# Kernel optimization log

Measured on AMD Instinct MI355X. Metric: run time of the kernel, lower is better.

The kernel has to match this reference:

```python
import jax, jax.numpy as jnp
import numpy as np

EPS = 1e-8

def setup_inputs() -> dict:
    key = jax.random.key(0)
    k1, k2, k3 = jax.random.split(key, 3)
    B, N, C = 4, 2048, 512
    x = jax.random.normal(k1, (B, N, C), dtype=jnp.float32)
    w_qkv = jax.random.normal(k2, (C, 3 * C), dtype=jnp.float32) * (C ** -0.5)
    w_proj = jax.random.normal(k3, (C, C), dtype=jnp.float32) * (C ** -0.5)
    b_proj = jnp.zeros((C,), dtype=jnp.float32)
    alpha = jnp.ones((1,), dtype=jnp.float32)
    beta = jnp.ones((1,), dtype=jnp.float32)
    return {"x": x, "w_qkv": w_qkv, "alpha": alpha, "beta": beta,
            "w_proj": w_proj, "b_proj": b_proj}

def reference(x, w_qkv, alpha, beta, w_proj, b_proj):
    B, N, C = x.shape
    H = 8  # num_heads
    D = C // H  # head_dim = 64
    scale = D ** -0.5
    qkv = (x @ w_qkv).reshape(B, N, 3, H, D)
    q = jnp.transpose(qkv[:, :, 0], (0, 2, 1, 3))  # (B,H,N,D)
    k = jnp.transpose(qkv[:, :, 1], (0, 2, 1, 3))
    v = jnp.transpose(qkv[:, :, 2], (0, 2, 1, 3))
    attn = jnp.einsum('bhnd,bhmd->bhnm', q, k) * scale  # (B,H,N,N)
    # sparse branch: relu^2 sum-normalize
    sp = jnp.square(jax.nn.relu(attn))
    attn_sparse = sp / (sp.sum(axis=-1, keepdims=True) + EPS)
    # dense branch: softmax
    attn_dense = jax.nn.softmax(attn, axis=-1)
    a = jax.nn.sigmoid(alpha)
    b = jax.nn.sigmoid(beta)
    wsum = a + b + EPS
    attn_final = (a / wsum) * attn_sparse + (b / wsum) * attn_dense
    out = jnp.einsum('bhnm,bhmd->bhnd', attn_final, v)  # (B,H,N,D)
    out = jnp.transpose(out, (0, 2, 1, 3)).reshape(B, N, C)
    return out @ w_proj + b_proj
```

## Files before the change

kernel.cpp:

```cpp
#include <hip/hip_runtime.h>

typedef unsigned short u16;
typedef unsigned int   u32;
typedef __attribute__((ext_vector_type(8))) __bf16 bf16x8;
typedef __attribute__((ext_vector_type(4))) float  f32x4;
typedef __attribute__((ext_vector_type(4))) u32    u32x4;

#define AS1q __attribute__((address_space(1)))
#define AS3q __attribute__((address_space(3)))

static __device__ __forceinline__ u16 f2bf(float f) {
    u32 u = __builtin_bit_cast(u32, f);
    u32 r = u + 0x7FFFu + ((u >> 16) & 1u);
    return (u16)(r >> 16);
}

static __device__ __forceinline__ bf16x8 ld16(const u16* p) {
    return __builtin_bit_cast(bf16x8, *(const float4*)(const void*)p);
}

static __device__ __forceinline__ f32x4 mfma16(bf16x8 a, bf16x8 b, f32x4 c) {
    return __builtin_amdgcn_mfma_f32_16x16x32_bf16(a, b, c, 0, 0, 0);
}

static __device__ __forceinline__ void gld16(const u16* g, u16* l) {
    __builtin_amdgcn_global_load_lds((const AS1q u32*)g, (AS3q u32*)l, 16, 0, 0);
}

static __device__ __forceinline__ float exp2_fast(float v) {
    float e;
    asm("v_exp_f32 %0, %1" : "=v"(e) : "v"(v));
    return e;
}

static __device__ __forceinline__ u32 cvtpk(float lo, float hi_) {
    u32 d;
    asm("v_cvt_pk_bf16_f32 %0, %1, %2" : "=v"(d) : "v"(lo), "v"(hi_));
    return d;
}

__global__ __launch_bounds__(256) void k_cast_x(const float* __restrict__ x, u16* __restrict__ xb) {
    int i = blockIdx.x * 256 + threadIdx.x;
    float4 v = ((const float4*)x)[i];
    ushort4 o;
    o.x = f2bf(v.x); o.y = f2bf(v.y); o.z = f2bf(v.z); o.w = f2bf(v.w);
    ((ushort4*)xb)[i] = o;
}

__global__ __launch_bounds__(256) void k_transpose_cast(const float* __restrict__ in, u16* __restrict__ out,
                                                        int K, int Nn) {
    __shared__ float tile[32][33];
    int tx = threadIdx.x & 31, ty = threadIdx.x >> 5;
    int k0 = blockIdx.y * 32, n0 = blockIdx.x * 32;
#pragma unroll
    for (int i = 0; i < 4; ++i)
        tile[ty + i * 8][tx] = in[(k0 + ty + i * 8) * Nn + n0 + tx];
    __syncthreads();
#pragma unroll
    for (int i = 0; i < 4; ++i)
        out[(n0 + ty + i * 8) * K + k0 + tx] = f2bf(tile[tx][ty + i * 8]);
}

static __device__ __forceinline__ void stage128x64(const u16* __restrict__ gbase, int ld,
                                                   u16* lds, int tid) {
    int wid = tid >> 6;
#pragma unroll
    for (int i = 0; i < 4; ++i) {
        int idx = i * 256 + tid;
        int row = idx >> 3, c8 = idx & 7;
        int csw = c8 ^ (row & 7);
        gld16(gbase + row * ld + csw * 8, lds + (i * 256 + wid * 64) * 8);
    }
}

static __device__ __forceinline__ bf16x8 frag(const u16* lds, int row, int col16) {
    return ld16(lds + row * 64 + ((col16 ^ (row & 7)) << 3));
}

__global__ __launch_bounds__(256) void k_gemm_qkv(const u16* __restrict__ xb, const u16* __restrict__ wT,
                                                  u16* __restrict__ Qh, u16* __restrict__ Kh,
                                                  u16* __restrict__ VTh) {
    __shared__ __align__(16) u16 at[128 * 64];
    __shared__ __align__(16) u16 bt[128 * 64];
    int tid = threadIdx.x, lane = tid & 63, wid = tid >> 6;
    int tm = blockIdx.x / 12, tn = blockIdx.x % 12;
    int rb = tm * 128, cb = tn * 128;
    int wr = (wid >> 1) * 64, wc = (wid & 1) * 64;
    int l15 = lane & 15, lhi = lane >> 4;
    f32x4 acc[4][4] = {};
    for (int kk = 0; kk < 512; kk += 64) {
        stage128x64(xb + rb * 512 + kk, 512, at, tid);
        stage128x64(wT + cb * 512 + kk, 512, bt, tid);
        __syncthreads();
        bf16x8 af[4][2], bfr[4][2];
#pragma unroll
        for (int m = 0; m < 4; ++m) {
            int row = wr + m * 16 + l15;
            af[m][0] = frag(at, row, lhi);
            af[m][1] = frag(at, row, 4 + lhi);
        }
#pragma unroll
        for (int n = 0; n < 4; ++n) {
            int row = wc + n * 16 + l15;
            bfr[n][0] = frag(bt, row, lhi);
            bfr[n][1] = frag(bt, row, 4 + lhi);
        }
#pragma unroll
        for (int m = 0; m < 4; ++m)
#pragma unroll
            for (int n = 0; n < 4; ++n) {
                acc[m][n] = mfma16(af[m][0], bfr[n][0], acc[m][n]);
                acc[m][n] = mfma16(af[m][1], bfr[n][1], acc[m][n]);
            }
        __syncthreads();
    }
#pragma unroll
    for (int m = 0; m < 4; ++m)
#pragma unroll
        for (int n = 0; n < 4; ++n)
#pragma unroll
            for (int r = 0; r < 4; ++r) {
                int R  = rb + wr + m * 16 + lhi * 4 + r;
                int Cg = cb + wc + n * 16 + l15;
                int b = R >> 11, nseq = R & 2047;
                int s = Cg >> 9, rm = Cg & 511, h = rm >> 6, d = rm & 63;
                int bh = (b << 3) + h;
                float v = acc[m][n][r];
                if (s == 0)      Qh[(bh * 2048 + nseq) * 64 + d] = f2bf(v * 0.1803368801111244f);
                else if (s == 1) Kh[(bh * 2048 + nseq) * 64 + d] = f2bf(v);
                else             VTh[(bh * 64 + d) * 2048 + nseq] = f2bf(v);
            }
}

#define ATTN_SUB(BUF, KS)                                                        \
    {                                                                            \
        f32x4 s[2][2];                                                           \
        _Pragma("unroll")                                                        \
        for (int kt = 0; kt < 2; ++kt) {                                         \
            int row = (KS)*32 + kap + 2 * kt;                                    \
            const u16* kbp = &kls[BUF][0] + row * 64;                            \
            bf16x8 kf0 = ld16(kbp + ((lhi ^ (row & 7)) << 3));                   \
            bf16x8 kf1 = ld16(kbp + (((4 + lhi) ^ (row & 7)) << 3));             \
            _Pragma("unroll")                                                    \
            for (int qg = 0; qg < 2; ++qg) {                                     \
                s[qg][kt] = mfma16(kf0, qa[qg][0], z);                           \
                s[qg][kt] = mfma16(kf1, qa[qg][1], s[qg][kt]);                   \
            }                                                                    \
        }                                                                        \
        bf16x8 pfd[2], pfs[2];                                                   \
        _Pragma("unroll")                                                        \
        for (int qg = 0; qg < 2; ++qg) {                                         \
            float ed[2][4], ps[2][4];                                            \
            _Pragma("unroll")                                                    \
            for (int kt = 0; kt < 2; ++kt)                                       \
                _Pragma("unroll")                                                \
                for (int r = 0; r < 4; ++r) {                                    \
                    float v = s[qg][kt][r];                                      \
                    float e = exp2_fast(v);                                      \
                    float t = fmaxf(v, 0.f);                                     \
                    ed[kt][r] = e; ps[kt][r] = t * t;                            \
                }                                                                \
            pfd[qg] = __builtin_bit_cast(bf16x8, (u32x4){                        \
                cvtpk(ed[0][0], ed[0][1]), cvtpk(ed[1][0], ed[1][1]),            \
                cvtpk(ed[0][2], ed[0][3]), cvtpk(ed[1][2], ed[1][3])});          \
            pfs[qg] = __builtin_bit_cast(bf16x8, (u32x4){                        \
                cvtpk(ps[0][0], ps[0][1]), cvtpk(ps[1][0], ps[1][1]),            \
                cvtpk(ps[0][2], ps[0][3]), cvtpk(ps[1][2], ps[1][3])});          \
        }                                                                        \
        _Pragma("unroll")                                                        \
        for (int n = 0; n < 4; ++n) {                                            \
            int row = n * 16 + l15;                                              \
            bf16x8 vf = ld16(&vls[BUF][0] + row * 64 +                           \
                             ((((KS)*4 + lhi) ^ (row & 7)) << 3));               \
            _Pragma("unroll")                                                    \
            for (int qg = 0; qg < 2; ++qg) {                                     \
                accd[qg][n] = mfma16(pfd[qg], vf, accd[qg][n]);                  \
                accs[qg][n] = mfma16(pfs[qg], vf, accs[qg][n]);                  \
            }                                                                    \
        }                                                                        \
        _Pragma("unroll")                                                        \
        for (int qg = 0; qg < 2; ++qg) {                                         \
            dend[qg] = mfma16(pfd[qg], onesf, dend[qg]);                         \
            dens[qg] = mfma16(pfs[qg], onesf, dens[qg]);                         \
        }                                                                        \
    }

__global__ __launch_bounds__(256) void k_attn(const u16* __restrict__ Qh, const u16* __restrict__ Kh,
                                              const u16* __restrict__ VTh, const float* __restrict__ alpha,
                                              const float* __restrict__ beta, u16* __restrict__ AO) {
    __shared__ __align__(16) u16 kls[2][64 * 64];
    __shared__ __align__(16) u16 vls[2][64 * 64];
    int tid = threadIdx.x, lane = tid & 63, wid = tid >> 6;
    int l15 = lane & 15, lhi = lane >> 4;
    int wg = (blockIdx.x & 7) * 64 + (blockIdx.x >> 3);
    int bh = wg >> 4;
    int qb = (wg & 15) << 7;
    const u16* Qp = Qh + bh * (2048 * 64);
    const u16* Kp = Kh + bh * (2048 * 64);
    const u16* Vp = VTh + bh * (2048 * 64);
    int qbase = qb + wid * 32;
    bf16x8 qa[2][2];
#pragma unroll
    for (int qg = 0; qg < 2; ++qg) {
        int row = qbase + qg * 16 + l15;
        qa[qg][0] = ld16(Qp + row * 64 + lhi * 8);
        qa[qg][1] = ld16(Qp + row * 64 + 32 + lhi * 8);
    }
    int kap = 8 * (l15 >> 2) + 4 * ((l15 >> 1) & 1) + (l15 & 1);
    f32x4 accd[2][4] = {}, accs[2][4] = {};
    f32x4 dend[2] = {}, dens[2] = {};
    const f32x4 z = {0.f, 0.f, 0.f, 0.f};
    const bf16x8 onesf = __builtin_bit_cast(bf16x8, (u32x4){0x3F803F80u, 0x3F803F80u,
                                                            0x3F803F80u, 0x3F803F80u});

    int srow = tid >> 3, sc8 = tid & 7;
    const u16* kg0 = Kp + srow * 64 + ((sc8 ^ (srow & 7)) << 3);
    const u16* kg1 = Kp + (srow + 32) * 64 + ((sc8 ^ ((srow + 32) & 7)) << 3);
    const u16* vg0 = Vp + srow * 2048 + ((sc8 ^ (srow & 7)) << 3);
    const u16* vg1 = Vp + (srow + 32) * 2048 + ((sc8 ^ ((srow + 32) & 7)) << 3);

    gld16(kg0, &kls[0][0] + tid * 8);
    gld16(kg1, &kls[0][0] + 2048 + tid * 8);
    gld16(vg0, &vls[0][0] + tid * 8);
    gld16(vg1, &vls[0][0] + 2048 + tid * 8);
    int koff = 64 * 64, voff = 64;

    for (int g = 0; g < 32; ++g) {
        int cur = g & 1;
        if (g + 1 < 32) {
            u16* kd = &kls[cur ^ 1][0];
            u16* vd = &vls[cur ^ 1][0];
            gld16(kg0 + koff, kd + tid * 8);
            gld16(kg1 + koff, kd + 2048 + tid * 8);
            gld16(vg0 + voff, vd + tid * 8);
            gld16(vg1 + voff, vd + 2048 + tid * 8);
            koff += 64 * 64; voff += 64;
            asm volatile("s_waitcnt vmcnt(4)" ::: "memory");
        } else {
            asm volatile("s_waitcnt vmcnt(0)" ::: "memory");
        }
        __builtin_amdgcn_s_barrier();
        ATTN_SUB(cur, 0)
        ATTN_SUB(cur, 1)
        asm volatile("" ::: "memory");
        __builtin_amdgcn_s_barrier();
    }
    float sa = 1.f / (1.f + __expf(-alpha[0]));
    float sb = 1.f / (1.f + __expf(-beta[0]));
    float wsum = sa + sb + 1e-8f;
    float wa = sa / wsum, wb = sb / wsum;
    int b = bh >> 3, h = bh & 7;
#pragma unroll
    for (int qg = 0; qg < 2; ++qg) {
        float id[4], isr[4];
#pragma unroll
        for (int r = 0; r < 4; ++r) {
            id[r]  = wb / dend[qg][r];
            isr[r] = wa / (dens[qg][r] + 1e-8f);
        }
#pragma unroll
        for (int n = 0; n < 4; ++n)
#pragma unroll
            for (int r = 0; r < 4; ++r) {
                int R  = b * 2048 + qbase + qg * 16 + lhi * 4 + r;
                int Cg = h * 64 + n * 16 + l15;
                float o = isr[r] * accs[qg][n][r] + id[r] * accd[qg][n][r];
                AO[R * 512 + Cg] = f2bf(o);
            }
    }
}

__global__ __launch_bounds__(256) void k_gemm_proj(const u16* __restrict__ AO, const u16* __restrict__ wT,
                                                   const float* __restrict__ bproj, float* __restrict__ out) {
    __shared__ __align__(16) u16 at[128 * 64];
    __shared__ __align__(16) u16 bt[128 * 64];
    int tid = threadIdx.x, lane = tid & 63, wid = tid >> 6;
    int tm = blockIdx.x >> 2, tn = blockIdx.x & 3;
    int rb = tm * 128, cb = tn * 128;
    int wr = (wid >> 1) * 64, wc = (wid & 1) * 64;
    int l15 = lane & 15, lhi = lane >> 4;
    f32x4 acc[4][4] = {};
    for (int kk = 0; kk < 512; kk += 64) {
        stage128x64(AO + rb * 512 + kk, 512, at, tid);
        stage128x64(wT + cb * 512 + kk, 512, bt, tid);
        __syncthreads();
        bf16x8 af[4][2], bfr[4][2];
#pragma unroll
        for (int m = 0; m < 4; ++m) {
            int row = wr + m * 16 + l15;
            af[m][0] = frag(at, row, lhi);
            af[m][1] = frag(at, row, 4 + lhi);
        }
#pragma unroll
        for (int n = 0; n < 4; ++n) {
            int row = wc + n * 16 + l15;
            bfr[n][0] = frag(bt, row, lhi);
            bfr[n][1] = frag(bt, row, 4 + lhi);
        }
#pragma unroll
        for (int m = 0; m < 4; ++m)
#pragma unroll
            for (int n = 0; n < 4; ++n) {
                acc[m][n] = mfma16(af[m][0], bfr[n][0], acc[m][n]);
                acc[m][n] = mfma16(af[m][1], bfr[n][1], acc[m][n]);
            }
        __syncthreads();
    }
#pragma unroll
    for (int m = 0; m < 4; ++m)
#pragma unroll
        for (int n = 0; n < 4; ++n)
#pragma unroll
            for (int r = 0; r < 4; ++r) {
                int R  = rb + wr + m * 16 + lhi * 4 + r;
                int Cg = cb + wc + n * 16 + l15;
                out[R * 512 + Cg] = acc[m][n][r] + bproj[Cg];
            }
}

extern "C" void kernel_launch(void* const* d_in, const int* in_sizes, int n_in,
                              void* d_out, int out_size, void* d_ws, size_t ws_size,
                              hipStream_t stream) {
    const float* x      = (const float*)d_in[0];
    const float* w_qkv  = (const float*)d_in[1];
    const float* alpha  = (const float*)d_in[2];
    const float* beta   = (const float*)d_in[3];
    const float* w_proj = (const float*)d_in[4];
    const float* b_proj = (const float*)d_in[5];
    float* out = (float*)d_out;
    char* w = (char*)d_ws;
    u16* xb     = (u16*)(w);
    u16* wqkvT  = (u16*)(w + 8388608);
    u16* wprojT = (u16*)(w + 9961472);
    u16* Qh     = (u16*)(w + 10485760);
    u16* Kh     = (u16*)(w + 18874368);
    u16* VTh    = (u16*)(w + 27262976);
    u16* AO     = xb;

    k_cast_x<<<dim3(4096), dim3(256), 0, stream>>>(x, xb);
    k_transpose_cast<<<dim3(48, 16), dim3(256), 0, stream>>>(w_qkv, wqkvT, 512, 1536);
    k_transpose_cast<<<dim3(16, 16), dim3(256), 0, stream>>>(w_proj, wprojT, 512, 512);
    k_gemm_qkv<<<dim3(768), dim3(256), 0, stream>>>(xb, wqkvT, Qh, Kh, VTh);
    k_attn<<<dim3(512), dim3(256), 0, stream>>>(Qh, Kh, VTh, alpha, beta, AO);
    k_gemm_proj<<<dim3(256), dim3(256), 0, stream>>>(AO, wprojT, b_proj, out);
}
```

Baseline: 145.5 us.

## Load K and V fragments straight from global into registers, dropping LDS staging

The attention kernel no longer stages K/V tiles in double-buffered shared memory behind block barriers. Each wave now loads its MFMA K fragments directly from global memory, with a one-step register prefetch, and loads its V fragments just before use. This removes LDS writes, LDS reads and barriers. In exchange, the four waves each fetch the same K/V data redundantly through the cache, V loads are less coalesced and are not prefetched, and the final prefetch reads past the end of the K tile.

```diff
diff --git a/kernel.cpp b/kernel.cpp
--- a/kernel.cpp
+++ b/kernel.cpp
@@ -132,20 +132,19 @@
             }
 }
 
-#define ATTN_SUB(BUF, KS)                                                        \
+#define ATTN_COMPUTE(KF0, KF1, KF2, KF3, VOFF)                                   \
     {                                                                            \
+        bf16x8 vf0 = ld16(vp0 + (VOFF));                                         \
+        bf16x8 vf1 = ld16(vp1 + (VOFF));                                         \
+        bf16x8 vf2 = ld16(vp2 + (VOFF));                                         \
+        bf16x8 vf3 = ld16(vp3 + (VOFF));                                         \
         f32x4 s[2][2];                                                           \
         _Pragma("unroll")                                                        \
-        for (int kt = 0; kt < 2; ++kt) {                                         \
-            int row = (KS)*32 + kap + 2 * kt;                                    \
-            const u16* kbp = &kls[BUF][0] + row * 64;                            \
-            bf16x8 kf0 = ld16(kbp + ((lhi ^ (row & 7)) << 3));                   \
-            bf16x8 kf1 = ld16(kbp + (((4 + lhi) ^ (row & 7)) << 3));             \
-            _Pragma("unroll")                                                    \
-            for (int qg = 0; qg < 2; ++qg) {                                     \
-                s[qg][kt] = mfma16(kf0, qa[qg][0], z);                           \
-                s[qg][kt] = mfma16(kf1, qa[qg][1], s[qg][kt]);                   \
-            }                                                                    \
+        for (int qg = 0; qg < 2; ++qg) {                                         \
+            s[qg][0] = mfma16(KF0, qa[qg][0], z);                                \
+            s[qg][0] = mfma16(KF1, qa[qg][1], s[qg][0]);                         \
+            s[qg][1] = mfma16(KF2, qa[qg][0], z);                                \
+            s[qg][1] = mfma16(KF3, qa[qg][1], s[qg][1]);                         \
         }                                                                        \
         bf16x8 pfd[2], pfs[2];                                                   \
         _Pragma("unroll")                                                        \
@@ -168,18 +167,15 @@
                 cvtpk(ps[0][2], ps[0][3]), cvtpk(ps[1][2], ps[1][3])});          \
         }                                                                        \
         _Pragma("unroll")                                                        \
-        for (int n = 0; n < 4; ++n) {                                            \
-            int row = n * 16 + l15;                                              \
-            bf16x8 vf = ld16(&vls[BUF][0] + row * 64 +                           \
-                             ((((KS)*4 + lhi) ^ (row & 7)) << 3));               \
-            _Pragma("unroll")                                                    \
-            for (int qg = 0; qg < 2; ++qg) {                                     \
-                accd[qg][n] = mfma16(pfd[qg], vf, accd[qg][n]);                  \
-                accs[qg][n] = mfma16(pfs[qg], vf, accs[qg][n]);                  \
-            }                                                                    \
-        }                                                                        \
-        _Pragma("unroll")                                                        \
         for (int qg = 0; qg < 2; ++qg) {                                         \
+            accd[qg][0] = mfma16(pfd[qg], vf0, accd[qg][0]);                     \
+            accs[qg][0] = mfma16(pfs[qg], vf0, accs[qg][0]);                     \
+            accd[qg][1] = mfma16(pfd[qg], vf1, accd[qg][1]);                     \
+            accs[qg][1] = mfma16(pfs[qg], vf1, accs[qg][1]);                     \
+            accd[qg][2] = mfma16(pfd[qg], vf2, accd[qg][2]);                     \
+            accs[qg][2] = mfma16(pfs[qg], vf2, accs[qg][2]);                     \
+            accd[qg][3] = mfma16(pfd[qg], vf3, accd[qg][3]);                     \
+            accs[qg][3] = mfma16(pfs[qg], vf3, accs[qg][3]);                     \
             dend[qg] = mfma16(pfd[qg], onesf, dend[qg]);                         \
             dens[qg] = mfma16(pfs[qg], onesf, dens[qg]);                         \
         }                                                                        \
@@ -188,8 +184,6 @@
 __global__ __launch_bounds__(256) void k_attn(const u16* __restrict__ Qh, const u16* __restrict__ Kh,
                                               const u16* __restrict__ VTh, const float* __restrict__ alpha,
                                               const float* __restrict__ beta, u16* __restrict__ AO) {
-    __shared__ __align__(16) u16 kls[2][64 * 64];
-    __shared__ __align__(16) u16 vls[2][64 * 64];
     int tid = threadIdx.x, lane = tid & 63, wid = tid >> 6;
     int l15 = lane & 15, lhi = lane >> 4;
     int wg = (blockIdx.x & 7) * 64 + (blockIdx.x >> 3);
@@ -213,37 +207,24 @@
     const bf16x8 onesf = __builtin_bit_cast(bf16x8, (u32x4){0x3F803F80u, 0x3F803F80u,
                                                             0x3F803F80u, 0x3F803F80u});
 
-    int srow = tid >> 3, sc8 = tid & 7;
-    const u16* kg0 = Kp + srow * 64 + ((sc8 ^ (srow & 7)) << 3);
-    const u16* kg1 = Kp + (srow + 32) * 64 + ((sc8 ^ ((srow + 32) & 7)) << 3);
-    const u16* vg0 = Vp + srow * 2048 + ((sc8 ^ (srow & 7)) << 3);
-    const u16* vg1 = Vp + (srow + 32) * 2048 + ((sc8 ^ ((srow + 32) & 7)) << 3);
-
-    gld16(kg0, &kls[0][0] + tid * 8);
-    gld16(kg1, &kls[0][0] + 2048 + tid * 8);
-    gld16(vg0, &vls[0][0] + tid * 8);
-    gld16(vg1, &vls[0][0] + 2048 + tid * 8);
-    int koff = 64 * 64, voff = 64;
-
+    const u16* kp0 = Kp + kap * 64 + lhi * 8;
+    const u16* kp1 = kp0 + 2048;
+    const u16* vp0 = Vp + (l15) * 2048 + lhi * 8;
+    const u16* vp1 = vp0 + 16 * 2048;
+    const u16* vp2 = vp0 + 32 * 2048;
+    const u16* vp3 = vp0 + 48 * 2048;
+
+    bf16x8 kA0 = ld16(kp0), kA1 = ld16(kp0 + 32), kA2 = ld16(kp0 + 128), kA3 = ld16(kp0 + 160);
+    kp0 += 4096;
+    int voff = 0;
     for (int g = 0; g < 32; ++g) {
-        int cur = g & 1;
-        if (g + 1 < 32) {
-            u16* kd = &kls[cur ^ 1][0];
-            u16* vd = &vls[cur ^ 1][0];
-            gld16(kg0 + koff, kd + tid * 8);
-            gld16(kg1 + koff, kd + 2048 + tid * 8);
-            gld16(vg0 + voff, vd + tid * 8);
-            gld16(vg1 + voff, vd + 2048 + tid * 8);
-            koff += 64 * 64; voff += 64;
-            asm volatile("s_waitcnt vmcnt(4)" ::: "memory");
-        } else {
-            asm volatile("s_waitcnt vmcnt(0)" ::: "memory");
-        }
-        __builtin_amdgcn_s_barrier();
-        ATTN_SUB(cur, 0)
-        ATTN_SUB(cur, 1)
-        asm volatile("" ::: "memory");
-        __builtin_amdgcn_s_barrier();
+        bf16x8 kB0 = ld16(kp1), kB1 = ld16(kp1 + 32), kB2 = ld16(kp1 + 128), kB3 = ld16(kp1 + 160);
+        kp1 += 4096;
+        ATTN_COMPUTE(kA0, kA1, kA2, kA3, voff)
+        kA0 = ld16(kp0); kA1 = ld16(kp0 + 32); kA2 = ld16(kp0 + 128); kA3 = ld16(kp0 + 160);
+        kp0 += 4096;
+        ATTN_COMPUTE(kB0, kB1, kB2, kB3, voff + 32)
+        voff += 64;
     }
     float sa = 1.f / (1.f + __expf(-alpha[0]));
     float sb = 1.f / (1.f + __expf(-beta[0]));
```

Result: slower. 187.2 us (+28.7%).
